# Performance work log

Hardware: AMD Instinct MI355X
Metric: run time of the kernel (lower is better)

Reference implementation:

```python
import jax, jax.numpy as jnp
import numpy as np

EPS = 1e-12  # torch F.normalize eps


def _l2_normalize(x, axis=-1):
    n = jnp.linalg.norm(x, axis=axis, keepdims=True)
    return x / jnp.maximum(n, EPS)


def setup_inputs() -> dict:
    key = jax.random.key(0)
    k1, k2 = jax.random.split(key)
    B, N, D, V = 4, 512, 768, 50257
    return {
        "query": jax.random.normal(k1, (B, N, D), dtype=jnp.float32),
        "key_embeddings": jax.random.normal(k2, (V, D), dtype=jnp.float32),
        "alpha_raw": jnp.float32(0.5),  # learnable scalar parameter (init_alpha)
        "k": 64,
    }


def reference(query, key_embeddings, alpha_raw, k):
    # query: [B,N,D], key_embeddings: [V,D]
    query_norm = _l2_normalize(query)            # [B,N,D]
    key_norm = _l2_normalize(key_embeddings)     # [V,D]
    # node-level cosine similarity, max-pooled over nodes
    node_sim = jnp.einsum('bnd,vd->bnv', query_norm, key_norm)  # [B,N,V]
    node_sim_pool = node_sim.max(axis=1)                        # [B,V]
    # graph-level similarity from mean of normalized node features
    graph_query = query_norm.mean(axis=1)                       # [B,D]
    graph_sim = jnp.einsum('bd,vd->bv', graph_query, key_norm)  # [B,V]
    alpha = jax.nn.sigmoid(alpha_raw)
    fused_similarity = alpha * node_sim_pool + (1.0 - alpha) * graph_sim  # [B,V]
    _, topk_indices = jax.lax.top_k(fused_similarity, k)        # [B,k]
    selected_keys = key_embeddings[topk_indices]                # [B,k,D]
    return selected_keys, topk_indices, fused_similarity, alpha
```

## Files before the change

### kernel.cpp

```cpp
#include <hip/hip_runtime.h>
#include <hip/hip_bf16.h>
#include <math.h>

#define D 768
#define BQ 4
#define NQ 512
#define M_TOTAL (BQ*NQ)
#define KSEL 64

typedef short bf16x8 __attribute__((ext_vector_type(8)));
typedef float f32x4  __attribute__((ext_vector_type(4)));

__device__ __forceinline__ void split1(float x, unsigned int& h, unsigned int& l)
{
    unsigned int u  = __float_as_uint(x);
    unsigned int hb = (u + 0x7fffu + ((u >> 16) & 1u)) & 0xffff0000u;
    h = hb >> 16;
    l = __float_as_uint(x - __uint_as_float(hb)) >> 16;
}


__global__ void split_invnorm_kernel(const float* __restrict__ x, unsigned short* __restrict__ sp,
                                     float* __restrict__ inv, int rows_src, int rows_dst)
{
    int r    = (blockIdx.x * blockDim.x + threadIdx.x) >> 6;
    int lane = threadIdx.x & 63;
    if (r >= rows_dst) return;
    int src = r < rows_src ? r : rows_src - 1;
    const float* row = x + (size_t)src * D;
    unsigned short* dh = sp + (size_t)r * (2*D);
    unsigned short* dl = dh + D;
    float ss = 0.f;
    #pragma unroll
    for (int s = 0; s < 3; ++s) {
        float4 v = *reinterpret_cast<const float4*>(row + s*256 + lane*4);
        ss += v.x*v.x + v.y*v.y + v.z*v.z + v.w*v.w;
        unsigned int h0,h1,h2,h3,l0,l1,l2,l3;
        split1(v.x,h0,l0); split1(v.y,h1,l1); split1(v.z,h2,l2); split1(v.w,h3,l3);
        ushort4 hv = make_ushort4((unsigned short)h0,(unsigned short)h1,(unsigned short)h2,(unsigned short)h3);
        ushort4 lv = make_ushort4((unsigned short)l0,(unsigned short)l1,(unsigned short)l2,(unsigned short)l3);
        *reinterpret_cast<ushort4*>(dh + s*256 + lane*4) = hv;
        *reinterpret_cast<ushort4*>(dl + s*256 + lane*4) = lv;
    }
    #pragma unroll
    for (int off = 32; off > 0; off >>= 1)
        ss += __shfl_xor(ss, off, 64);
    if (lane == 0 && r < rows_src)
        inv[r] = 1.0f / fmaxf(sqrtf(ss), 1e-12f);
}

#define GBM 256
#define GBN 128
#define GBK 32
#define GNT (D/GBK)
#define SLOT_A 32768
#define SLOT_SZ 49152

__device__ __forceinline__ void gload16(const unsigned short* g, char* l)
{
    __builtin_amdgcn_global_load_lds((const __attribute__((address_space(1))) void*)g,
                                     (__attribute__((address_space(3))) void*)l, 16, 0, 0);
}

__global__ __launch_bounds__(512, 2)
void fast_gemm(const unsigned short* __restrict__ Qsp, const unsigned short* __restrict__ Ksp,
               const float* __restrict__ invq, float* __restrict__ pmax, float* __restrict__ psum,
               int Vp, int gx)
{
    extern __shared__ char smem[];

    const int t    = threadIdx.x;
    const int lane = t & 63;
    const int w    = t >> 6;
    const int wr   = w >> 1;
    const int wc   = w & 1;

    int lid = blockIdx.x;
    int u   = (lid & 7) * gx + (lid >> 3);
    const int by = u & 7;
    const int bx = u >> 3;
    const int m0 = by * GBM;
    const int v0 = bx * GBN;

    const int lrow = lane >> 3;
    const int cc   = (lane & 7) ^ lrow;
    const size_t goff = (size_t)lrow * (2*D) + (size_t)(cc >> 2) * D + (size_t)(cc & 3) * 8;

    const unsigned short* gA = Qsp + (size_t)m0 * (2*D) + goff;
    const unsigned short* gB = Ksp + (size_t)v0 * (2*D) + goff;

    #define STAGE_FULL(k0_, slot_) do {                                   \
        const unsigned short* ga_ = gA + (k0_);                           \
        char* la_ = (slot_);                                              \
        _Pragma("unroll")                                                 \
        for (int j = 0; j < 4; ++j) {                                     \
            int ii = (w << 2) + j;                                        \
            gload16(ga_ + (size_t)ii * 8 * (2*D), la_ + ii*1024);         \
        }                                                                 \
        const unsigned short* gb_ = gB + (k0_);                           \
        char* lb_ = (slot_) + SLOT_A;                                     \
        _Pragma("unroll")                                                 \
        for (int j = 0; j < 2; ++j) {                                     \
            int ii = (w << 1) + j;                                        \
            gload16(gb_ + (size_t)ii * 8 * (2*D), lb_ + ii*1024);         \
        }                                                                 \
    } while (0)

    #define STAGE_A2(k0_, slot_, j0_) do { if (st_) {                     \
        const unsigned short* ga_ = gA + (k0_);                           \
        char* la_ = (slot_);                                              \
        int ii0 = (w << 2) + (j0_);                                       \
        gload16(ga_ + (size_t)ii0 * 8 * (2*D), la_ + ii0*1024);           \
        int ii1 = ii0 + 1;                                                \
        gload16(ga_ + (size_t)ii1 * 8 * (2*D), la_ + ii1*1024);           \
    } } while (0)

    #define STAGE_B1(k0_, slot_, j_) do { if (st_) {                      \
        const unsigned short* gb_ = gB + (k0_);                           \
        char* lb_ = (slot_) + SLOT_A;                                     \
        int ii = (w << 1) + (j_);                                         \
        gload16(gb_ + (size_t)ii * 8 * (2*D), lb_ + ii*1024);             \
    } } while (0)

    const int l15 = lane & 15, kg = lane >> 4;
    const int swz_hi = ((kg)     ^ (lane & 7)) * 16;
    const int swz_lo = ((4 + kg) ^ (lane & 7)) * 16;
    const int offAhi = (wr*64 + l15)*128 + swz_hi;
    const int offAlo = (wr*64 + l15)*128 + swz_lo;
    const int offBhi = (wc*64 + l15)*128 + swz_hi;
    const int offBlo = (wc*64 + l15)*128 + swz_lo;

    f32x4 acc[4][4];
    #pragma unroll
    for (int i = 0; i < 4; ++i)
        #pragma unroll
        for (int j = 0; j < 4; ++j)
            acc[i][j] = f32x4{0.f,0.f,0.f,0.f};

    char* s0 = smem;
    char* s1 = smem + SLOT_SZ;
    char* s2 = smem + 2*SLOT_SZ;
    STAGE_FULL(0,   s0);
    STAGE_FULL(GBK, s1);
    char *sc = s0, *sn = s1, *ss = s2;

    for (int T = 0; T < GNT; ++T) {
        const bool st_ = (T + 2 < GNT);
        const int  k2  = (T + 2) * GBK;
        const char* sA_ = sc;
        const char* sB_ = sc + SLOT_A;

        if (T < GNT - 1) asm volatile("s_waitcnt vmcnt(6)" ::: "memory");
        else             asm volatile("s_waitcnt vmcnt(0)" ::: "memory");
        __builtin_amdgcn_s_barrier();

        bf16x8 Bh[4], Bl[4];
        #pragma unroll
        for (int f = 0; f < 4; ++f) {
            Bh[f] = *(const bf16x8*)(sB_ + offBhi + f*2048);
            Bl[f] = *(const bf16x8*)(sB_ + offBlo + f*2048);
        }
        bf16x8 Ah = *(const bf16x8*)(sA_ + offAhi);
        bf16x8 Al = *(const bf16x8*)(sA_ + offAlo);
        STAGE_A2(k2, ss, 0);
        __builtin_amdgcn_s_barrier();
        asm volatile("s_waitcnt lgkmcnt(0)" ::: "memory");
        __builtin_amdgcn_s_setprio(1);
        #pragma unroll
        for (int fn = 0; fn < 4; ++fn) {
            acc[0][fn] = __builtin_amdgcn_mfma_f32_16x16x32_bf16(Ah, Bh[fn], acc[0][fn], 0,0,0);
            acc[0][fn] = __builtin_amdgcn_mfma_f32_16x16x32_bf16(Ah, Bl[fn], acc[0][fn], 0,0,0);
            acc[0][fn] = __builtin_amdgcn_mfma_f32_16x16x32_bf16(Al, Bh[fn], acc[0][fn], 0,0,0);
        }
        __builtin_amdgcn_s_setprio(0);
        __builtin_amdgcn_s_barrier();

        #pragma unroll
        for (int p = 1; p < 4; ++p) {
            Ah = *(const bf16x8*)(sA_ + offAhi + p*2048);
            Al = *(const bf16x8*)(sA_ + offAlo + p*2048);
            if (p == 1)      STAGE_A2(k2, ss, 2);
            else if (p == 2) STAGE_B1(k2, ss, 0);
            else             STAGE_B1(k2, ss, 1);
            __builtin_amdgcn_s_barrier();
            asm volatile("s_waitcnt lgkmcnt(0)" ::: "memory");
            __builtin_amdgcn_s_setprio(1);
            #pragma unroll
            for (int fn = 0; fn < 4; ++fn) {
                acc[p][fn] = __builtin_amdgcn_mfma_f32_16x16x32_bf16(Ah, Bh[fn], acc[p][fn], 0,0,0);
                acc[p][fn] = __builtin_amdgcn_mfma_f32_16x16x32_bf16(Ah, Bl[fn], acc[p][fn], 0,0,0);
                acc[p][fn] = __builtin_amdgcn_mfma_f32_16x16x32_bf16(Al, Bh[fn], acc[p][fn], 0,0,0);
            }
            __builtin_amdgcn_s_setprio(0);
            __builtin_amdgcn_s_barrier();
        }
        char* tmp = sc; sc = sn; sn = ss; ss = tmp;
    }
    #undef STAGE_FULL
    #undef STAGE_A2
    #undef STAGE_B1

    float iq[16];
    #pragma unroll
    for (int fm = 0; fm < 4; ++fm)
        #pragma unroll
        for (int r = 0; r < 4; ++r)
            iq[fm*4+r] = invq[m0 + wr*64 + fm*16 + kg*4 + r];

    float* redm = (float*)smem;
    float* reds = redm + 512;
    #pragma unroll
    for (int fn = 0; fn < 4; ++fn) {
        float pmv = -INFINITY, psv = 0.f;
        #pragma unroll
        for (int fm = 0; fm < 4; ++fm)
            #pragma unroll
            for (int r = 0; r < 4; ++r) {
                float x = acc[fm][fn][r] * iq[fm*4+r];
                pmv = fmaxf(pmv, x);
                psv += x;
            }
        pmv = fmaxf(pmv, __shfl_xor(pmv, 16, 64));
        pmv = fmaxf(pmv, __shfl_xor(pmv, 32, 64));
        psv += __shfl_xor(psv, 16, 64);
        psv += __shfl_xor(psv, 32, 64);
        if (lane < 16) {
            redm[wr*128 + wc*64 + fn*16 + l15] = pmv;
            reds[wr*128 + wc*64 + fn*16 + l15] = psv;
        }
    }
    __syncthreads();
    if (t < 128) {
        float m01 = fmaxf(redm[t], redm[128+t]);
        float m23 = fmaxf(redm[256+t], redm[384+t]);
        float sm  = reds[t] + reds[128+t] + reds[256+t] + reds[384+t];
        pmax[(size_t)by * Vp + v0 + t] = fmaxf(m01, m23);
        psum[(size_t)by * Vp + v0 + t] = sm;
    }
}

__global__ void blend_kernel(const float* __restrict__ pmax, const float* __restrict__ psum,
                             const float* __restrict__ invk, const float* __restrict__ alpha_raw,
                             float* __restrict__ out_fused, float* __restrict__ out_alpha,
                             int V, int Vp)
{
    int v = blockIdx.x * 256 + threadIdx.x;
    float alpha = 1.0f / (1.0f + expf(-alpha_raw[0]));
    if (blockIdx.x == 0 && threadIdx.x == 0) out_alpha[0] = alpha;
    if (v >= V) return;
    float ik = invk[v];
    #pragma unroll
    for (int b = 0; b < BQ; ++b) {
        float nm = fmaxf(pmax[(size_t)(2*b)*Vp + v], pmax[(size_t)(2*b+1)*Vp + v]) * ik;
        float gs = (psum[(size_t)(2*b)*Vp + v] + psum[(size_t)(2*b+1)*Vp + v]) * ik * (1.0f/(float)NQ);
        out_fused[(size_t)b*V + v] = alpha*nm + (1.0f-alpha)*gs;
    }
}

__device__ __forceinline__ unsigned int mono_map(float f)
{
    unsigned int u = __float_as_uint(f);
    return u ^ ((u & 0x80000000u) ? 0xFFFFFFFFu : 0x80000000u);
}

__global__ __launch_bounds__(1024)
void topk_radix_kernel(const float* __restrict__ fused,
                       int* __restrict__ idxout, float* __restrict__ out_idx, int V)
{
    const int b = blockIdx.x, t = threadIdx.x;
    const float* row = fused + (size_t)b * V;

    __shared__ unsigned int hist[256];
    __shared__ unsigned int sh_pref;
    __shared__ int sh_kneed;
    __shared__ unsigned int sh_nA, sh_nE;
    __shared__ unsigned long long key[64];
    __shared__ int eqIdx[256];

    unsigned int pref = 0;
    int kneed = KSEL;
    #pragma unroll
    for (int p = 24; p >= 0; p -= 8) {
        if (t < 256) hist[t] = 0;
        __syncthreads();
        unsigned int mask = (p == 24) ? 0u : (0xFFFFFFFFu << (p + 8));
        for (int i = t; i < V; i += 1024) {
            unsigned int u = mono_map(row[i]);
            if ((u & mask) == pref)
                atomicAdd(&hist[(u >> p) & 255u], 1u);
        }
        __syncthreads();
        if (t == 0) {
            int cum = 0, sel = 0;
            for (int bb = 255; bb >= 0; --bb) {
                int c = (int)hist[bb];
                if (cum + c >= kneed) { sel = bb; break; }
                cum += c;
            }
            sh_pref  = pref | ((unsigned int)sel << p);
            sh_kneed = kneed - cum;
        }
        __syncthreads();
        pref  = sh_pref;
        kneed = sh_kneed;
        __syncthreads();
    }

    const unsigned int T = pref;
    if (t == 0) { sh_nA = 0; sh_nE = 0; }
    __syncthreads();
    for (int i = t; i < V; i += 1024) {
        unsigned int u = mono_map(row[i]);
        if (u > T) {
            unsigned int pos = atomicAdd(&sh_nA, 1u);
            if (pos < 64) key[pos] = ((unsigned long long)(~u) << 32) | (unsigned int)i;
        } else if (u == T) {
            unsigned int pos = atomicAdd(&sh_nE, 1u);
            if (pos < 256) eqIdx[pos] = i;
        }
    }
    __syncthreads();
    const int nA = (int)sh_nA;
    const int nE = (int)sh_nE;
    if (t < 256 && t >= min(nE, 256)) eqIdx[t] = 0x7fffffff;
    __syncthreads();
    if (nE > 1) {
        for (int k = 2; k <= 256; k <<= 1)
            for (int j = k >> 1; j > 0; j >>= 1) {
                if (t < 256) {
                    int ixj = t ^ j;
                    if (ixj > t) {
                        int a = eqIdx[t], c = eqIdx[ixj];
                        bool up = ((t & k) == 0);
                        if ((a > c) == up) { eqIdx[t] = c; eqIdx[ixj] = a; }
                    }
                }
                __syncthreads();
            }
    }
    if (t < kneed)
        key[nA + t] = ((unsigned long long)(~T) << 32) | (unsigned int)eqIdx[t];
    __syncthreads();
    for (int k = 2; k <= 64; k <<= 1)
        for (int j = k >> 1; j > 0; j >>= 1) {
            if (t < 64) {
                int ixj = t ^ j;
                if (ixj > t) {
                    unsigned long long a = key[t], c = key[ixj];
                    bool up = ((t & k) == 0);
                    if ((a > c) == up) { key[t] = c; key[ixj] = a; }
                }
            }
            __syncthreads();
        }
    if (t < KSEL) {
        int idx = (int)(unsigned int)(key[t] & 0xFFFFFFFFull);
        idxout[b*KSEL + t]  = idx;
        out_idx[b*KSEL + t] = (float)idx;
    }
}

__global__ void gather_kernel(const int* __restrict__ idx, const float* __restrict__ Kmat,
                              float* __restrict__ out_sel)
{
    int j = blockIdx.x & 63, b = blockIdx.x >> 6, t = threadIdx.x;
    int sel = idx[b*KSEL + j];
    float4 v = *reinterpret_cast<const float4*>(Kmat + (size_t)sel * D + t*4);
    *reinterpret_cast<float4*>(out_sel + ((size_t)(b*KSEL + j)) * D + t*4) = v;
}

#define BMT 128
#define BVT 128
#define NSTEP (D/32)

__global__ void row_invnorm_kernel(const float* __restrict__ x, float* __restrict__ inv, int rows)
{
    int wid  = (blockIdx.x * blockDim.x + threadIdx.x) >> 6;
    int lane = threadIdx.x & 63;
    if (wid >= rows) return;
    const float* r = x + (size_t)wid * D;
    float ss = 0.f;
    #pragma unroll
    for (int s = 0; s < 3; ++s) {
        float4 v = *reinterpret_cast<const float4*>(r + s*256 + lane*4);
        ss += v.x*v.x + v.y*v.y + v.z*v.z + v.w*v.w;
    }
    #pragma unroll
    for (int off = 32; off > 0; off >>= 1)
        ss += __shfl_xor(ss, off, 64);
    if (lane == 0) inv[wid] = 1.0f / fmaxf(sqrtf(ss), 1e-12f);
}

__global__ void compute_gq_kernel(const float* __restrict__ q, const float* __restrict__ invq,
                                  float* __restrict__ gq)
{
    int t = blockIdx.x * blockDim.x + threadIdx.x;
    if (t >= BQ*D) return;
    int b = t / D, d = t - b*D;
    float acc = 0.f;
    const float* qb = q + (size_t)b * NQ * D + d;
    const float* iq = invq + b*NQ;
    for (int n = 0; n < NQ; ++n)
        acc += iq[n] * qb[(size_t)n*D];
    gq[t] = acc * (1.0f/(float)NQ);
}

__device__ __forceinline__ void split8(float4 a, float4 b, uint4& hi, uint4& lo)
{
    unsigned int h0,h1,h2,h3,h4,h5,h6,h7, l0,l1,l2,l3,l4,l5,l6,l7;
    split1(a.x,h0,l0); split1(a.y,h1,l1); split1(a.z,h2,l2); split1(a.w,h3,l3);
    split1(b.x,h4,l4); split1(b.y,h5,l5); split1(b.z,h6,l6); split1(b.w,h7,l7);
    hi.x = h0 | (h1<<16); hi.y = h2 | (h3<<16); hi.z = h4 | (h5<<16); hi.w = h6 | (h7<<16);
    lo.x = l0 | (l1<<16); lo.y = l2 | (l3<<16); lo.z = l4 | (l5<<16); lo.w = l6 | (l7<<16);
}

__global__ __launch_bounds__(256)
void mfma_gemm_maxpool(const float* __restrict__ Q, const float* __restrict__ Kmat,
                       const float* __restrict__ invq, const float* __restrict__ invk,
                       float* __restrict__ partial, int V, int Vp)
{
    __shared__ __align__(16) unsigned short lds[16384];
    const int t    = threadIdx.x;
    const int lane = t & 63;
    const int w    = t >> 6;
    const int wr   = w >> 1;
    const int wc   = w & 1;
    const int v0   = blockIdx.x * BVT;
    const int m0   = blockIdx.y * BMT;

    const int srow = t >> 1;
    const int scol = (t & 1) * 16;
    const int c0   = (t & 1) * 2;
    const unsigned int ps0 = (c0     + (srow >> 1)) & 3;
    const unsigned int ps1 = (c0 + 1 + (srow >> 1)) & 3;
    const unsigned int wO0 = srow*32 + ps0*8;
    const unsigned int wO1 = srow*32 + ps1*8;

    const float* Ap = Q + (size_t)(m0 + srow) * D + scol;
    int vrow = v0 + srow; if (vrow > V-1) vrow = V-1;
    const float* Bp = Kmat + (size_t)vrow * D + scol;

    const int lr = lane & 15, kg = lane >> 4;
    const int arowb = wr*64 + lr;
    const int browb = wc*64 + lr;
    const unsigned int slotA = (kg + (arowb >> 1)) & 3;
    const unsigned int slotB = (kg + (browb >> 1)) & 3;
    const unsigned int offA = arowb*32 + slotA*8;
    const unsigned int offB = browb*32 + slotB*8;

    f32x4 acc[4][4];
    #pragma unroll
    for (int i = 0; i < 4; ++i)
        #pragma unroll
        for (int j = 0; j < 4; ++j)
            acc[i][j] = f32x4{0.f,0.f,0.f,0.f};

    float4 ra0,ra1,ra2,ra3, rb0,rb1,rb2,rb3;
    #define LOADSTEP(s_) do { \
        const float* ap_ = Ap + (s_)*32; const float* bp_ = Bp + (s_)*32; \
        ra0 = *(const float4*)(ap_);    ra1 = *(const float4*)(ap_+4); \
        ra2 = *(const float4*)(ap_+8);  ra3 = *(const float4*)(ap_+12); \
        rb0 = *(const float4*)(bp_);    rb1 = *(const float4*)(bp_+4); \
        rb2 = *(const float4*)(bp_+8);  rb3 = *(const float4*)(bp_+12); \
    } while(0)

    LOADSTEP(0);
    for (int s = 0; s < NSTEP; ++s) {
        uint4 ah0,al0, ah1,al1, bh0,bl0, bh1,bl1;
        split8(ra0,ra1, ah0,al0); split8(ra2,ra3, ah1,al1);
        split8(rb0,rb1, bh0,bl0); split8(rb2,rb3, bh1,bl1);
        __syncthreads();
        *(uint4*)&lds[        wO0] = ah0;  *(uint4*)&lds[ 4096 + wO0] = al0;
        *(uint4*)&lds[        wO1] = ah1;  *(uint4*)&lds[ 4096 + wO1] = al1;
        *(uint4*)&lds[ 8192 + wO0] = bh0;  *(uint4*)&lds[12288 + wO0] = bl0;
        *(uint4*)&lds[ 8192 + wO1] = bh1;  *(uint4*)&lds[12288 + wO1] = bl1;
        if (s + 1 < NSTEP) LOADSTEP(s + 1);
        __syncthreads();

        bf16x8 Ah[4], Al[4], Bh[4], Bl[4];
        #pragma unroll
        for (int fm = 0; fm < 4; ++fm) {
            unsigned int o = offA + fm*512;
            Ah[fm] = *(const bf16x8*)&lds[o];
            Al[fm] = *(const bf16x8*)&lds[4096 + o];
        }
        #pragma unroll
        for (int fv = 0; fv < 4; ++fv) {
            unsigned int o = offB + fv*512;
            Bh[fv] = *(const bf16x8*)&lds[8192 + o];
            Bl[fv] = *(const bf16x8*)&lds[12288 + o];
        }
        #pragma unroll
        for (int fm = 0; fm < 4; ++fm)
            #pragma unroll
            for (int fv = 0; fv < 4; ++fv) {
                acc[fm][fv] = __builtin_amdgcn_mfma_f32_16x16x32_bf16(Ah[fm], Bh[fv], acc[fm][fv], 0,0,0);
                acc[fm][fv] = __builtin_amdgcn_mfma_f32_16x16x32_bf16(Ah[fm], Bl[fv], acc[fm][fv], 0,0,0);
                acc[fm][fv] = __builtin_amdgcn_mfma_f32_16x16x32_bf16(Al[fm], Bh[fv], acc[fm][fv], 0,0,0);
            }
    }
    #undef LOADSTEP

    __syncthreads();
    float* red = (float*)lds;
    float iq[4][4];
    #pragma unroll
    for (int fm = 0; fm < 4; ++fm)
        #pragma unroll
        for (int r = 0; r < 4; ++r)
            iq[fm][r] = invq[m0 + wr*64 + fm*16 + kg*4 + r];
    #pragma unroll
    for (int fv = 0; fv < 4; ++fv) {
        float tm = -INFINITY;
        #pragma unroll
        for (int fm = 0; fm < 4; ++fm)
            #pragma unroll
            for (int r = 0; r < 4; ++r)
                tm = fmaxf(tm, acc[fm][fv][r] * iq[fm][r]);
        tm = fmaxf(tm, __shfl_xor(tm, 16, 64));
        tm = fmaxf(tm, __shfl_xor(tm, 32, 64));
        if (lane < 16) red[wr*128 + wc*64 + fv*16 + lane] = tm;
    }
    __syncthreads();
    if (t < 128) {
        int v = v0 + t;
        if (v < V)
            partial[(size_t)blockIdx.y * Vp + v] = fmaxf(red[t], red[128 + t]) * invk[v];
    }
}

__global__ void fused_sim_kernel(const float* __restrict__ Kmat, const float* __restrict__ invk,
                                 const float* __restrict__ gq, const float* __restrict__ partial,
                                 const float* __restrict__ alpha_raw,
                                 float* __restrict__ out_fused, float* __restrict__ out_alpha,
                                 int V, int Vp)
{
    int wib  = threadIdx.x >> 6;
    int lane = threadIdx.x & 63;
    float alpha = 1.0f / (1.0f + expf(-alpha_raw[0]));
    if (blockIdx.x == 0 && threadIdx.x == 0) out_alpha[0] = alpha;
    int v = blockIdx.x * 4 + wib;
    if (v >= V) return;
    const float* kr = Kmat + (size_t)v * D;
    float accb[BQ] = {0.f,0.f,0.f,0.f};
    #pragma unroll
    for (int s = 0; s < 3; ++s) {
        float4 kv = *reinterpret_cast<const float4*>(kr + s*256 + lane*4);
        #pragma unroll
        for (int b = 0; b < BQ; ++b) {
            float4 gv = *reinterpret_cast<const float4*>(gq + b*D + s*256 + lane*4);
            accb[b] += gv.x*kv.x + gv.y*kv.y + gv.z*kv.z + gv.w*kv.w;
        }
    }
    #pragma unroll
    for (int b = 0; b < BQ; ++b)
        #pragma unroll
        for (int off = 32; off > 0; off >>= 1)
            accb[b] += __shfl_xor(accb[b], off, 64);
    if (lane < BQ) {
        int b = lane;
        float node = partial[(size_t)(b*4+0)*Vp + v];
        #pragma unroll
        for (int i = 1; i < 4; ++i)
            node = fmaxf(node, partial[(size_t)(b*4+i)*Vp + v]);
        float graph = accb[b] * invk[v];
        out_fused[(size_t)b*V + v] = alpha*node + (1.0f-alpha)*graph;
    }
}

__global__ __launch_bounds__(1024)
void topk_gather_kernel(const float* __restrict__ fused, const float* __restrict__ Kmat,
                        float* __restrict__ scratch, float* __restrict__ out_sel,
                        float* __restrict__ out_idx, int V, int Vp)
{
    const int b = blockIdx.x, t = threadIdx.x;
    const int lane = t & 63, wid = t >> 6;
    const float* row = fused + (size_t)b * V;
    float* s = scratch + (size_t)b * Vp;
    for (int i = t; i < V; i += 1024) s[i] = row[i];
    __syncthreads();

    const int CH = (V + 1023) / 1024;
    const int lo = t * CH;
    const int hi = min(V, lo + CH);
    float lmax = -INFINITY; int lidx = 0x7fffffff;
    for (int i = lo; i < hi; ++i) { float x = s[i]; if (x > lmax) { lmax = x; lidx = i; } }

    __shared__ float swv[16];
    __shared__ int   swi[16];
    __shared__ int   sbest;

    for (int j = 0; j < KSEL; ++j) {
        float v = lmax; int id = lidx;
        #pragma unroll
        for (int off = 32; off > 0; off >>= 1) {
            float ov = __shfl_xor(v, off, 64);
            int   oi = __shfl_xor(id, off, 64);
            if (ov > v || (ov == v && oi < id)) { v = ov; id = oi; }
        }
        if (lane == 0) { swv[wid] = v; swi[wid] = id; }
        __syncthreads();
        if (t == 0) {
            float bv = swv[0]; int bi = swi[0];
            for (int x = 1; x < 16; ++x)
                if (swv[x] > bv || (swv[x] == bv && swi[x] < bi)) { bv = swv[x]; bi = swi[x]; }
            sbest = bi;
            out_idx[b*KSEL + j] = (float)bi;
        }
        __syncthreads();
        const int sel = sbest;
        if (sel >= lo && sel < hi) {
            s[sel] = -INFINITY;
            lmax = -INFINITY; lidx = 0x7fffffff;
            for (int i = lo; i < hi; ++i) { float x = s[i]; if (x > lmax) { lmax = x; lidx = i; } }
        }
        if (t < 192) {
            float4 kv = *reinterpret_cast<const float4*>(&Kmat[(size_t)sel * D + t*4]);
            *reinterpret_cast<float4*>(&out_sel[((size_t)b*KSEL + j)*D + t*4]) = kv;
        }
        __syncthreads();
    }
}

extern "C" void kernel_launch(void* const* d_in, const int* in_sizes, int n_in,
                              void* d_out, int out_size, void* d_ws, size_t ws_size,
                              hipStream_t stream)
{
    const float* q         = (const float*)d_in[0];
    const float* kemb      = (const float*)d_in[1];
    const float* alpha_raw = (const float*)d_in[2];
    int V = in_sizes[1] / D;

    float* out_sel   = (float*)d_out;
    float* out_idx   = out_sel + BQ*KSEL*D;
    float* out_fused = out_idx + BQ*KSEL;
    float* out_alpha = out_fused + (size_t)BQ*V;

    size_t Vp = (size_t)((V + 255) & ~255);
    float* ws      = (float*)d_ws;
    float* invk    = ws;
    float* invq    = invk + Vp;
    float* pmax    = invq + M_TOTAL;
    float* psum    = pmax + 8*Vp;
    float* scratch = psum + 8*Vp;
    int*   idxbuf  = (int*)(scratch + 4*Vp);
    unsigned short* Qsp = (unsigned short*)(idxbuf + 256);
    unsigned short* Ksp = Qsp + (size_t)M_TOTAL * (2*D);
    size_t need = (size_t)((char*)(Ksp + Vp*(2*D)) - (char*)d_ws);

    if (ws_size >= need) {
        split_invnorm_kernel<<<M_TOTAL/4, 256, 0, stream>>>(q, Qsp, invq, M_TOTAL, M_TOTAL);
        split_invnorm_kernel<<<(int)(Vp/4), 256, 0, stream>>>(kemb, Ksp, invk, V, (int)Vp);

        hipFuncSetAttribute(reinterpret_cast<const void*>(fast_gemm),
                            hipFuncAttributeMaxDynamicSharedMemorySize, 3*SLOT_SZ);

        int gx = (int)(Vp / GBN);
        fast_gemm<<<gx*8, 512, 3*SLOT_SZ, stream>>>(Qsp, Ksp, invq, pmax, psum, (int)Vp, gx);

        blend_kernel<<<(V + 255)/256, 256, 0, stream>>>(pmax, psum, invk, alpha_raw,
                                                        out_fused, out_alpha, V, (int)Vp);
        topk_radix_kernel<<<BQ, 1024, 0, stream>>>(out_fused, idxbuf, out_idx, V);
        gather_kernel<<<BQ*KSEL, 192, 0, stream>>>(idxbuf, kemb, out_sel);
    } else {
        int Vp2 = (V + 127) & ~127;
        float* f_invk    = ws;
        float* f_invq    = f_invk + Vp2;
        float* f_gq      = f_invq + M_TOTAL;
        float* f_partial = f_gq + BQ*D;
        float* f_scratch = f_partial + (size_t)16*Vp2;

        row_invnorm_kernel<<<(V + 3)/4, 256, 0, stream>>>(kemb, f_invk, V);
        row_invnorm_kernel<<<(M_TOTAL + 3)/4, 256, 0, stream>>>(q, f_invq, M_TOTAL);
        compute_gq_kernel<<<(BQ*D + 255)/256, 256, 0, stream>>>(q, f_invq, f_gq);

        dim3 g(Vp2 / BVT, M_TOTAL / BMT);
        mfma_gemm_maxpool<<<g, 256, 0, stream>>>(q, kemb, f_invq, f_invk, f_partial, V, Vp2);

        fused_sim_kernel<<<(V + 3)/4, 256, 0, stream>>>(kemb, f_invk, f_gq, f_partial, alpha_raw,
                                                        out_fused, out_alpha, V, Vp2);
        topk_gather_kernel<<<BQ, 1024, 0, stream>>>(out_fused, kemb, f_scratch, out_sel, out_idx, V, Vp2);
    }
}
```

Baseline: 566.5 us.

## Widen GEMM tile to 256x256 with double-buffered LDS and 2x4 warp grid

The split-bf16 GEMM tile grows from 256x128 to 256x256, and warps are rearranged into a 2x4 grid where each warp computes 128x64. This raises arithmetic intensity and halves the number of blocks and the global reloads of the Q tiles. The LDS pipeline drops from three stages to two 64KB slots, with loads staged per phase and new vmcnt waits. The cost is more accumulator registers per thread (32 f32x4) and less prefetch depth, so occupancy or latency hiding may suffer.

```diff
diff --git a/kernel.cpp b/kernel.cpp
--- a/kernel.cpp
+++ b/kernel.cpp
@@ -50,11 +50,11 @@
 }
 
 #define GBM 256
-#define GBN 128
+#define GBN 256
 #define GBK 32
 #define GNT (D/GBK)
-#define SLOT_A 32768
-#define SLOT_SZ 49152
+#define SLOT_B_OFF 32768
+#define SLOT_SZ 65536
 
 __device__ __forceinline__ void gload16(const unsigned short* g, char* l)
 {
@@ -72,8 +72,8 @@
     const int t    = threadIdx.x;
     const int lane = t & 63;
     const int w    = t >> 6;
-    const int wr   = w >> 1;
-    const int wc   = w & 1;
+    const int wr   = w >> 2;
+    const int wc   = w & 3;
 
     int lid = blockIdx.x;
     int u   = (lid & 7) * gx + (lid >> 3);
@@ -86,137 +86,109 @@
     const int cc   = (lane & 7) ^ lrow;
     const size_t goff = (size_t)lrow * (2*D) + (size_t)(cc >> 2) * D + (size_t)(cc & 3) * 8;
 
-    const unsigned short* gA = Qsp + (size_t)m0 * (2*D) + goff;
-    const unsigned short* gB = Ksp + (size_t)v0 * (2*D) + goff;
-
-    #define STAGE_FULL(k0_, slot_) do {                                   \
-        const unsigned short* ga_ = gA + (k0_);                           \
-        char* la_ = (slot_);                                              \
-        _Pragma("unroll")                                                 \
-        for (int j = 0; j < 4; ++j) {                                     \
-            int ii = (w << 2) + j;                                        \
-            gload16(ga_ + (size_t)ii * 8 * (2*D), la_ + ii*1024);         \
-        }                                                                 \
-        const unsigned short* gb_ = gB + (k0_);                           \
-        char* lb_ = (slot_) + SLOT_A;                                     \
-        _Pragma("unroll")                                                 \
-        for (int j = 0; j < 2; ++j) {                                     \
-            int ii = (w << 1) + j;                                        \
-            gload16(gb_ + (size_t)ii * 8 * (2*D), lb_ + ii*1024);         \
-        }                                                                 \
-    } while (0)
-
-    #define STAGE_A2(k0_, slot_, j0_) do { if (st_) {                     \
-        const unsigned short* ga_ = gA + (k0_);                           \
-        char* la_ = (slot_);                                              \
-        int ii0 = (w << 2) + (j0_);                                       \
-        gload16(ga_ + (size_t)ii0 * 8 * (2*D), la_ + ii0*1024);           \
-        int ii1 = ii0 + 1;                                                \
-        gload16(ga_ + (size_t)ii1 * 8 * (2*D), la_ + ii1*1024);           \
-    } } while (0)
-
-    #define STAGE_B1(k0_, slot_, j_) do { if (st_) {                      \
-        const unsigned short* gb_ = gB + (k0_);                           \
-        char* lb_ = (slot_) + SLOT_A;                                     \
-        int ii = (w << 1) + (j_);                                         \
-        gload16(gb_ + (size_t)ii * 8 * (2*D), lb_ + ii*1024);             \
-    } } while (0)
+    const int rAbase = ((w & 3) << 3) + ((w >> 2) << 7);
+    const int rBbase = w * 32;
+
+    const unsigned short* gAsrc = Qsp + (size_t)(m0 + rAbase) * (2*D) + goff;
+    const unsigned short* gBsrc = Ksp + (size_t)(v0 + rBbase) * (2*D) + goff;
+
+    #define SAk(k_, sl_, j_) gload16(gAsrc + (k_) + (size_t)(j_)*32*(2*D), (sl_) + (rAbase + (j_)*32)*128)
+    #define SBk(k_, sl_, j_) gload16(gBsrc + (k_) + (size_t)(j_)*8 *(2*D), (sl_) + SLOT_B_OFF + (rBbase + (j_)*8)*128)
 
     const int l15 = lane & 15, kg = lane >> 4;
-    const int swz_hi = ((kg)     ^ (lane & 7)) * 16;
-    const int swz_lo = ((4 + kg) ^ (lane & 7)) * 16;
-    const int offAhi = (wr*64 + l15)*128 + swz_hi;
-    const int offAlo = (wr*64 + l15)*128 + swz_lo;
-    const int offBhi = (wc*64 + l15)*128 + swz_hi;
-    const int offBlo = (wc*64 + l15)*128 + swz_lo;
-
-    f32x4 acc[4][4];
-    #pragma unroll
-    for (int i = 0; i < 4; ++i)
+    const int sHi = ((kg    ) ^ (lane & 7)) * 16;
+    const int sLo = ((kg + 4) ^ (lane & 7)) * 16;
+    const int offA = (wr*128 + l15) * 128;
+    const int offB = SLOT_B_OFF + (wc*64 + l15) * 128;
+
+    f32x4 acc[8][4];
+    #pragma unroll
+    for (int i = 0; i < 8; ++i)
         #pragma unroll
         for (int j = 0; j < 4; ++j)
             acc[i][j] = f32x4{0.f,0.f,0.f,0.f};
 
-    char* s0 = smem;
-    char* s1 = smem + SLOT_SZ;
-    char* s2 = smem + 2*SLOT_SZ;
-    STAGE_FULL(0,   s0);
-    STAGE_FULL(GBK, s1);
-    char *sc = s0, *sn = s1, *ss = s2;
+    bf16x8 Bh[4], Bl[4];
+
+    char* sl0 = smem;
+    char* sl1 = smem + SLOT_SZ;
+
+    SBk(0, sl0, 0); SBk(0, sl0, 1); SAk(0, sl0, 0);
+    SBk(0, sl0, 2); SBk(0, sl0, 3); SAk(0, sl0, 1);
+    SAk(0, sl0, 2); SAk(0, sl0, 3);
+    asm volatile("s_waitcnt vmcnt(2)" ::: "memory");
+    __builtin_amdgcn_s_barrier();
+
+    #define PHASE(p_, STG, VMW) do {                                                         \
+        bf16x8 Ah0 = *(const bf16x8*)(scur + offA + (2*(p_)  )*2048 + sHi);                  \
+        bf16x8 Al0 = *(const bf16x8*)(scur + offA + (2*(p_)  )*2048 + sLo);                  \
+        bf16x8 Ah1 = *(const bf16x8*)(scur + offA + (2*(p_)+1)*2048 + sHi);                  \
+        bf16x8 Al1 = *(const bf16x8*)(scur + offA + (2*(p_)+1)*2048 + sLo);                  \
+        STG;                                                                                 \
+        __builtin_amdgcn_s_barrier();                                                        \
+        asm volatile("s_waitcnt lgkmcnt(0)" ::: "memory");                                   \
+        __builtin_amdgcn_s_setprio(1);                                                       \
+        _Pragma("unroll")                                                                    \
+        for (int nf = 0; nf < 4; ++nf) {                                                     \
+            acc[2*(p_)  ][nf] = __builtin_amdgcn_mfma_f32_16x16x32_bf16(Ah0, Bh[nf], acc[2*(p_)  ][nf], 0,0,0); \
+            acc[2*(p_)+1][nf] = __builtin_amdgcn_mfma_f32_16x16x32_bf16(Ah1, Bh[nf], acc[2*(p_)+1][nf], 0,0,0); \
+        }                                                                                    \
+        _Pragma("unroll")                                                                    \
+        for (int nf = 0; nf < 4; ++nf) {                                                     \
+            acc[2*(p_)  ][nf] = __builtin_amdgcn_mfma_f32_16x16x32_bf16(Ah0, Bl[nf], acc[2*(p_)  ][nf], 0,0,0); \
+            acc[2*(p_)+1][nf] = __builtin_amdgcn_mfma_f32_16x16x32_bf16(Ah1, Bl[nf], acc[2*(p_)+1][nf], 0,0,0); \
+        }                                                                                    \
+        _Pragma("unroll")                                                                    \
+        for (int nf = 0; nf < 4; ++nf) {                                                     \
+            acc[2*(p_)  ][nf] = __builtin_amdgcn_mfma_f32_16x16x32_bf16(Al0, Bh[nf], acc[2*(p_)  ][nf], 0,0,0); \
+            acc[2*(p_)+1][nf] = __builtin_amdgcn_mfma_f32_16x16x32_bf16(Al1, Bh[nf], acc[2*(p_)+1][nf], 0,0,0); \
+        }                                                                                    \
+        __builtin_amdgcn_s_setprio(0);                                                       \
+        VMW;                                                                                 \
+        __builtin_amdgcn_s_barrier();                                                        \
+    } while(0)
 
     for (int T = 0; T < GNT; ++T) {
-        const bool st_ = (T + 2 < GNT);
-        const int  k2  = (T + 2) * GBK;
-        const char* sA_ = sc;
-        const char* sB_ = sc + SLOT_A;
-
-        if (T < GNT - 1) asm volatile("s_waitcnt vmcnt(6)" ::: "memory");
-        else             asm volatile("s_waitcnt vmcnt(0)" ::: "memory");
-        __builtin_amdgcn_s_barrier();
-
-        bf16x8 Bh[4], Bl[4];
-        #pragma unroll
-        for (int f = 0; f < 4; ++f) {
-            Bh[f] = *(const bf16x8*)(sB_ + offBhi + f*2048);
-            Bl[f] = *(const bf16x8*)(sB_ + offBlo + f*2048);
-        }
-        bf16x8 Ah = *(const bf16x8*)(sA_ + offAhi);
-        bf16x8 Al = *(const bf16x8*)(sA_ + offAlo);
-        STAGE_A2(k2, ss, 0);
-        __builtin_amdgcn_s_barrier();
-        asm volatile("s_waitcnt lgkmcnt(0)" ::: "memory");
-        __builtin_amdgcn_s_setprio(1);
-        #pragma unroll
-        for (int fn = 0; fn < 4; ++fn) {
-            acc[0][fn] = __builtin_amdgcn_mfma_f32_16x16x32_bf16(Ah, Bh[fn], acc[0][fn], 0,0,0);
-            acc[0][fn] = __builtin_amdgcn_mfma_f32_16x16x32_bf16(Ah, Bl[fn], acc[0][fn], 0,0,0);
-            acc[0][fn] = __builtin_amdgcn_mfma_f32_16x16x32_bf16(Al, Bh[fn], acc[0][fn], 0,0,0);
-        }
-        __builtin_amdgcn_s_setprio(0);
-        __builtin_amdgcn_s_barrier();
-
-        #pragma unroll
-        for (int p = 1; p < 4; ++p) {
-            Ah = *(const bf16x8*)(sA_ + offAhi + p*2048);
-            Al = *(const bf16x8*)(sA_ + offAlo + p*2048);
-            if (p == 1)      STAGE_A2(k2, ss, 2);
-            else if (p == 2) STAGE_B1(k2, ss, 0);
-            else             STAGE_B1(k2, ss, 1);
-            __builtin_amdgcn_s_barrier();
-            asm volatile("s_waitcnt lgkmcnt(0)" ::: "memory");
-            __builtin_amdgcn_s_setprio(1);
-            #pragma unroll
-            for (int fn = 0; fn < 4; ++fn) {
-                acc[p][fn] = __builtin_amdgcn_mfma_f32_16x16x32_bf16(Ah, Bh[fn], acc[p][fn], 0,0,0);
-                acc[p][fn] = __builtin_amdgcn_mfma_f32_16x16x32_bf16(Ah, Bl[fn], acc[p][fn], 0,0,0);
-                acc[p][fn] = __builtin_amdgcn_mfma_f32_16x16x32_bf16(Al, Bh[fn], acc[p][fn], 0,0,0);
-            }
-            __builtin_amdgcn_s_setprio(0);
-            __builtin_amdgcn_s_barrier();
-        }
-        char* tmp = sc; sc = sn; sn = ss; ss = tmp;
-    }
-    #undef STAGE_FULL
-    #undef STAGE_A2
-    #undef STAGE_B1
-
-    float iq[16];
-    #pragma unroll
-    for (int fm = 0; fm < 4; ++fm)
+        const bool st = (T + 1 < GNT);
+        char* scur = (T & 1) ? sl1 : sl0;
+        char* snxt = (T & 1) ? sl0 : sl1;
+        const int k1 = (T + 1) * GBK;
+
+        #pragma unroll
+        for (int nf = 0; nf < 4; ++nf) {
+            Bh[nf] = *(const bf16x8*)(scur + offB + nf*2048 + sHi);
+            Bl[nf] = *(const bf16x8*)(scur + offB + nf*2048 + sLo);
+        }
+        PHASE(0, { if (st) { SBk(k1, snxt, 0); SBk(k1, snxt, 1); SAk(k1, snxt, 0); } }, );
+        PHASE(1, { if (st) { SBk(k1, snxt, 2); SBk(k1, snxt, 3); SAk(k1, snxt, 1); } },
+                 { if (st) asm volatile("s_waitcnt vmcnt(6)" ::: "memory");
+                   else    asm volatile("s_waitcnt vmcnt(0)" ::: "memory"); });
+        PHASE(2, { if (st) SAk(k1, snxt, 2); }, );
+        PHASE(3, { if (st) SAk(k1, snxt, 3); },
+                 { if (st) asm volatile("s_waitcnt vmcnt(2)" ::: "memory"); });
+    }
+    #undef PHASE
+    #undef SAk
+    #undef SBk
+
+    __syncthreads();
+    float iq[32];
+    #pragma unroll
+    for (int mf = 0; mf < 8; ++mf)
         #pragma unroll
         for (int r = 0; r < 4; ++r)
-            iq[fm*4+r] = invq[m0 + wr*64 + fm*16 + kg*4 + r];
+            iq[mf*4+r] = invq[m0 + wr*128 + mf*16 + kg*4 + r];
 
     float* redm = (float*)smem;
     float* reds = redm + 512;
     #pragma unroll
-    for (int fn = 0; fn < 4; ++fn) {
+    for (int nf = 0; nf < 4; ++nf) {
         float pmv = -INFINITY, psv = 0.f;
         #pragma unroll
-        for (int fm = 0; fm < 4; ++fm)
+        for (int mf = 0; mf < 8; ++mf)
             #pragma unroll
             for (int r = 0; r < 4; ++r) {
-                float x = acc[fm][fn][r] * iq[fm*4+r];
+                float x = acc[mf][nf][r] * iq[mf*4+r];
                 pmv = fmaxf(pmv, x);
                 psv += x;
             }
@@ -225,17 +197,14 @@
         psv += __shfl_xor(psv, 16, 64);
         psv += __shfl_xor(psv, 32, 64);
         if (lane < 16) {
-            redm[wr*128 + wc*64 + fn*16 + l15] = pmv;
-            reds[wr*128 + wc*64 + fn*16 + l15] = psv;
-        }
-    }
-    __syncthreads();
-    if (t < 128) {
-        float m01 = fmaxf(redm[t], redm[128+t]);
-        float m23 = fmaxf(redm[256+t], redm[384+t]);
-        float sm  = reds[t] + reds[128+t] + reds[256+t] + reds[384+t];
-        pmax[(size_t)by * Vp + v0 + t] = fmaxf(m01, m23);
-        psum[(size_t)by * Vp + v0 + t] = sm;
+            redm[wr*256 + wc*64 + nf*16 + l15] = pmv;
+            reds[wr*256 + wc*64 + nf*16 + l15] = psv;
+        }
+    }
+    __syncthreads();
+    if (t < 256) {
+        pmax[(size_t)by * Vp + v0 + t] = fmaxf(redm[t], redm[256+t]);
+        psum[(size_t)by * Vp + v0 + t] = reds[t] + reds[256+t];
     }
 }
 
@@ -653,10 +622,10 @@
         split_invnorm_kernel<<<(int)(Vp/4), 256, 0, stream>>>(kemb, Ksp, invk, V, (int)Vp);
 
         hipFuncSetAttribute(reinterpret_cast<const void*>(fast_gemm),
-                            hipFuncAttributeMaxDynamicSharedMemorySize, 3*SLOT_SZ);
+                            hipFuncAttributeMaxDynamicSharedMemorySize, 2*SLOT_SZ);
 
         int gx = (int)(Vp / GBN);
-        fast_gemm<<<gx*8, 512, 3*SLOT_SZ, stream>>>(Qsp, Ksp, invq, pmax, psum, (int)Vp, gx);
+        fast_gemm<<<gx*8, 512, 2*SLOT_SZ, stream>>>(Qsp, Ksp, invq, pmax, psum, (int)Vp, gx);
 
         blend_kernel<<<(V + 255)/256, 256, 0, stream>>>(pmax, psum, invk, alpha_raw,
                                                         out_fused, out_alpha, V, (int)Vp);
```

Measured after the change: 523.5 us. 7.6% less time.
